# Optimization experiments

Measured on AMD Instinct MI355X. Metric: run time of the kernel, lower is better.

Reference implementation:

```python
import jax, jax.numpy as jnp
import numpy as np

B, P, H, W = 8, 128, 32, 32
NC = 4                 # num_classes = NUM_REL_GROUP + 1
DOBJ = 4424            # 2*DOBJ = 8848
CIN = 256
C = 128 + 8848         # 8976 GCN channel dim


def setup_inputs() -> dict:
    key = jax.random.key(0)
    ks = jax.random.split(key, 24)
    s = 0.02  # weight scale to keep activations moderate
    inp = {
        "x": jax.random.normal(ks[0], (B, CIN, H, W), jnp.float32),
        "rel_pair_idxs": jax.random.randint(ks[1], (B, P, 2), 0, 640, dtype=jnp.int32),
        "obj_rep": jax.random.normal(ks[2], (640, DOBJ), jnp.float32),
        # ADD_GCN params
        "fc_w": jax.random.normal(ks[3], (NC, CIN), jnp.float32) * s,
        "ct_w": jax.random.normal(ks[4], (128, CIN), jnp.float32) * s,
        "ct_b": jnp.zeros((128,), jnp.float32),
        # DynamicGraphConvolution params
        "A": jax.random.normal(ks[5], (NC, NC), jnp.float32) * 0.25,          # static_adj conv1d (no bias)
        "sw_w": jax.random.normal(ks[6], (C, C), jnp.float32) * s / np.sqrt(C) * 30,
        "sw_b": jnp.zeros((C,), jnp.float32),
        "cg_w": jax.random.normal(ks[7], (C, C), jnp.float32) * s / np.sqrt(C) * 30,
        "cg_b": jnp.zeros((C,), jnp.float32),
        "bn_g": jnp.ones((C,), jnp.float32),
        "bn_b": jnp.zeros((C,), jnp.float32),
        "bn_m": jnp.zeros((C,), jnp.float32),
        "bn_v": jnp.ones((C,), jnp.float32),
        "co_w": jax.random.normal(ks[8], (NC, 2 * C), jnp.float32) * s / np.sqrt(C) * 30,
        "co_b": jnp.zeros((NC,), jnp.float32),
        "dw_w": jax.random.normal(ks[9], (C, C), jnp.float32) * s / np.sqrt(C) * 30,
        "dw_b": jnp.zeros((C,), jnp.float32),
        "ll_w": jax.random.normal(ks[10], (NC, C), jnp.float32) * s / np.sqrt(C) * 30,
        "ll_b": jnp.zeros((NC,), jnp.float32),
        "mask_mat": jnp.eye(NC, dtype=jnp.float32),
    }
    return inp


def reference(x, rel_pair_idxs, obj_rep, fc_w, ct_w, ct_b, A, sw_w, sw_b,
              cg_w, cg_b, bn_g, bn_b, bn_m, bn_v, co_w, co_b, dw_w, dw_b,
              ll_w, ll_b, mask_mat):
    leaky = lambda t: jax.nn.leaky_relu(t, 0.2)
    b, cin, h, w = x.shape
    xr = x.reshape(b, cin, h * w)                                  # (B,256,HW)

    # forward_classification_sm: fc -> topk(1).mean == max over spatial
    y = jnp.einsum('oc,bcs->bos', fc_w, xr)                        # (B,NC,HW)
    out1 = y.max(-1)                                               # (B,NC)

    # forward_sam
    mask = jax.nn.sigmoid(y)                                       # (B,NC,HW)
    v = jnp.einsum('oc,bcs->bos', ct_w, xr) + ct_b[None, :, None]  # (B,128,HW)
    v = jnp.einsum('bcs,bns->bcn', v, mask)                        # (B,128,NC)

    # pairwise object features (gather), tiled over NC node slots
    o1 = obj_rep[rel_pair_idxs[..., 0]]                            # (B,P,DOBJ)
    o2 = obj_rep[rel_pair_idxs[..., 1]]
    pf = jnp.concatenate([o1, o2], -1)                             # (B,P,8848)
    p = pf.shape[1]
    pf = jnp.broadcast_to(pf[..., None], pf.shape + (NC,))         # (B,P,8848,NC)
    vb = jnp.broadcast_to(v[:, None], (b, p) + v.shape[1:])        # (B,P,128,NC)
    g = jnp.concatenate([pf, vb], 2).reshape(b * p, C, NC)         # (BP,C,NC)

    # --- DynamicGraphConvolution ---
    # static GCN: node-mix conv1d (no bias) + leaky, then channel 1x1 conv + leaky
    xs = leaky(jnp.einsum('nm,pcm->pcn', A, g))                    # (BP,C,NC)
    xs = leaky(jnp.einsum('oc,pcn->pon', sw_w, xs) + sw_b[None, :, None])
    hg = g + xs

    # dynamic adjacency
    glb = hg.mean(-1)                                              # (BP,C) gap
    glb = glb @ cg_w.T + cg_b                                      # conv_global (1x1)
    glb = (glb - bn_m) * jax.lax.rsqrt(bn_v + 1e-5) * bn_g + bn_b  # BN (eval)
    glb = leaky(glb)
    # conv_create_co_mat over cat([glb_expand, hg], ch) without materializing cat
    adj = jax.nn.sigmoid(
        jnp.einsum('oc,pc->po', co_w[:, :C], glb)[:, :, None]
        + jnp.einsum('oc,pcn->pon', co_w[:, C:], hg)
        + co_b[None, :, None])                                     # (BP,NC,NC)

    # dynamic GCN
    hd = leaky(jnp.einsum('pcn,pnm->pcm', hg, adj))
    z = leaky(jnp.einsum('oc,pcn->pon', dw_w, hd) + dw_b[None, :, None])  # (BP,C,NC)

    # head: last_linear + leaky, masked diagonal sum
    out2 = leaky(jnp.einsum('oc,pcn->pon', ll_w, z) + ll_b[None, :, None])  # (BP,NC,NC)
    out2 = (out2 * jax.lax.stop_gradient(mask_mat)).sum(-1)        # (BP,NC)

    o1b = jnp.broadcast_to(out1[:, None], (b, p, NC)).reshape(b * p, NC)
    return ((o1b + out2) * 0.5).reshape(b, p, NC)
```

## Files before the change

### kernel.cpp

```cpp
#include <hip/hip_runtime.h>
#include <stdint.h>

#define DEVI __device__ __forceinline__

typedef unsigned short u16;
typedef __bf16 bf16x8 __attribute__((ext_vector_type(8)));
typedef float f32x4 __attribute__((ext_vector_type(4)));
typedef u16 u16x8 __attribute__((ext_vector_type(8)));

DEVI u16 f2bf(float f){
  union { float f; unsigned u; } v; v.f = f;
  unsigned r = v.u + 0x7FFFu + ((v.u >> 16) & 1u);
  return (u16)(r >> 16);
}
DEVI float bf2f(u16 h){
  union { unsigned u; float f; } v; v.u = ((unsigned)h) << 16;
  return v.f;
}
DEVI float lky(float t){ return t > 0.f ? t : 0.2f * t; }

#define GLD16(gp, lp) __builtin_amdgcn_global_load_lds( \
    (const __attribute__((address_space(1))) void*)(gp), \
    (__attribute__((address_space(3))) void*)(lp), 16, 0, 0)

template<int EPI>
__global__ __launch_bounds__(1024, 4)
void gemmU(const u16* __restrict__ A, const u16* __restrict__ B,
           int Kp, int Nt, int SN, int Mreal, float* __restrict__ C, long long ldc,
           const float* __restrict__ bias, const float* __restrict__ scale,
           const float* __restrict__ off, const float* __restrict__ llw,
           float* __restrict__ oacc)
{
  __shared__ __align__(16) u16 As[2][16384];
  __shared__ __align__(16) u16 Bs[2][16384];
  const int t    = threadIdx.x;
  const int lane = t & 63;
  const int wid  = t >> 6;
  const int wr = wid >> 2, wc = wid & 3;
  const int l4 = lane >> 4, l15 = lane & 15;

  const int nwg = gridDim.x;
  const int xc = blockIdx.x & 7, pp = blockIdx.x >> 3;
  const int qq = nwg >> 3, rr = nwg & 7;
  const int wg = (xc < rr ? xc*(qq+1) : rr*(qq+1) + (xc-rr)*qq) + pp;
  const int strip_sz = (nwg / Nt) * SN;
  const int strip = wg / strip_sz, srem = wg % strip_sz;
  const int mt = srem / SN, nt = strip*SN + srem % SN;

  const size_t am0 = (size_t)mt*256;
  const size_t bn0 = (size_t)nt*256;

  f32x4 acc[4][4];
  #pragma unroll
  for (int i = 0; i < 4; ++i)
    #pragma unroll
    for (int j = 0; j < 4; ++j) acc[i][j] = f32x4{0.f,0.f,0.f,0.f};
  bf16x8 afr[4], bfr[4];

  const int NT = Kp >> 6;

  const int srl0 = t >> 3, ssl = t & 7;
  const u16* pA = A + (am0 + srl0)*(size_t)Kp;
  const u16* pB = B + (bn0 + srl0)*(size_t)Kp;
  const size_t rowskip = (size_t)128 * Kp;
  const int sco0 = ((ssl ^ (srl0 & 7))*8);
  const int sco1 = ((ssl ^ ((srl0+128) & 7))*8);

  int aoff[4], boff[4];
  #pragma unroll
  for (int mi = 0; mi < 4; ++mi){
    const int r = wr*64 + mi*16 + l15;
    aoff[mi] = r*64 + ((r & 7)*8);
  }
  #pragma unroll
  for (int ni = 0; ni < 4; ++ni){
    const int r = wc*64 + ni*16 + l15;
    boff[ni] = r*64 + ((r & 7)*8);
  }

  auto STAGE = [&](int kc, int buf){
    u16* la = &As[buf][0]; u16* lb = &Bs[buf][0];
    GLD16(pA + kc + sco0,           la + t*8);
    GLD16(pA + rowskip + kc + sco1, la + 8192 + t*8);
    GLD16(pB + kc + sco0,           lb + t*8);
    GLD16(pB + rowskip + kc + sco1, lb + 8192 + t*8);
  };

  STAGE(0, 0);
  asm volatile("s_waitcnt vmcnt(0)" ::: "memory");
  __builtin_amdgcn_s_barrier();

  #define GU_BODY(KT, RB_, WB_)                                              \
  {                                                                          \
    const int nx = ((KT)+1 < NT) ? (KT)+1 : NT-1;                            \
    STAGE(nx*64, WB_);                                                       \
    const u16* ab = &As[RB_][0];                                             \
    const u16* bb = &Bs[RB_][0];                                             \
    _Pragma("unroll")                                                        \
    for (int ks = 0; ks < 2; ++ks){                                          \
      const int sx = (ks*4 + l4)*8;                                          \
      _Pragma("unroll")                                                      \
      for (int mi = 0; mi < 4; ++mi)                                         \
        afr[mi] = *(const bf16x8*)&ab[aoff[mi] ^ sx];                        \
      _Pragma("unroll")                                                      \
      for (int ni = 0; ni < 4; ++ni)                                         \
        bfr[ni] = *(const bf16x8*)&bb[boff[ni] ^ sx];                        \
      __builtin_amdgcn_s_setprio(1);                                         \
      _Pragma("unroll")                                                      \
      for (int mi = 0; mi < 4; ++mi)                                         \
        _Pragma("unroll")                                                    \
        for (int ni = 0; ni < 4; ++ni)                                       \
          acc[mi][ni] = __builtin_amdgcn_mfma_f32_16x16x32_bf16(             \
              afr[mi], bfr[ni], acc[mi][ni], 0, 0, 0);                       \
      __builtin_amdgcn_s_setprio(0);                                         \
    }                                                                        \
    asm volatile("s_waitcnt vmcnt(0)" ::: "memory");                         \
    __builtin_amdgcn_s_barrier();                                            \
  }

  for (int kt = 0; kt < NT; kt += 2){
    GU_BODY(kt,   0, 1);
    GU_BODY(kt+1, 1, 0);
  }
  #undef GU_BODY

  const int ob0 = mt*256 + wr*64;
  const int nb0 = nt*256 + wc*64;

  if (EPI == 0){
    #pragma unroll
    for (int mi = 0; mi < 4; ++mi){
      const int ob = ob0 + mi*16 + l4*4;
      if (ob < Mreal){
        #pragma unroll
        for (int ni = 0; ni < 4; ++ni){
          const int n = nb0 + ni*16 + l15;
          *(f32x4*)&C[(size_t)n*ldc + ob] = acc[mi][ni];
        }
      }
    }
  } else if (EPI == 2){
    #pragma unroll
    for (int mi = 0; mi < 4; ++mi){
      const int ob = ob0 + mi*16 + l4*4;
      if (ob < Mreal){
        const float sc0=scale[ob],sc1=scale[ob+1],sc2=scale[ob+2],sc3=scale[ob+3];
        const float of0=off[ob],of1=off[ob+1],of2=off[ob+2],of3=off[ob+3];
        #pragma unroll
        for (int ni = 0; ni < 4; ++ni){
          const int n = nb0 + ni*16 + l15;
          f32x4 a = acc[mi][ni];
          f32x4 vv = { lky(a[0]*sc0+of0), lky(a[1]*sc1+of1),
                       lky(a[2]*sc2+of2), lky(a[3]*sc3+of3) };
          *(f32x4*)&C[(size_t)n*ldc + ob] = vv;
        }
      }
    }
  } else {
    #pragma unroll
    for (int ni = 0; ni < 4; ++ni){
      float s0=0.f, s1=0.f, s2=0.f, s3=0.f;
      #pragma unroll
      for (int mi = 0; mi < 4; ++mi){
        #pragma unroll
        for (int r = 0; r < 4; ++r){
          const int o = ob0 + mi*16 + l4*4 + r;
          if (o < Mreal){
            const float val = lky(acc[mi][ni][r] + bias[o]);
            s0 += llw[o]         * val;
            s1 += llw[8976 + o]  * val;
            s2 += llw[17952 + o] * val;
            s3 += llw[26928 + o] * val;
          }
        }
      }
      const int n = nb0 + ni*16 + l15;
      const int q = n >> 2, m = n & 3;
      float sv[4] = {s0,s1,s2,s3};
      #pragma unroll
      for (int o4 = 0; o4 < 4; ++o4){
        float tt = sv[o4];
        tt += __shfl_xor(tt, 16);
        tt += __shfl_xor(tt, 32);
        if (l4 == 0) atomicAdd(&oacc[(q*4 + o4)*4 + m], tt);
      }
    }
  }
}

__global__ __launch_bounds__(256)
void gemm_vpre(const u16* __restrict__ A, const u16* __restrict__ B,
               int Kp, int Nt, int Mreal, float* __restrict__ C, long long ldc,
               const float* __restrict__ bias)
{
  __shared__ __align__(16) u16 As[2][4096];
  __shared__ __align__(16) u16 Bs[2][4096];
  const int tid  = threadIdx.x;
  const int lane = tid & 63;
  const int wr   = (tid >> 6) >> 1, wc = (tid >> 6) & 1;
  const int l4   = lane >> 4, l15 = lane & 15;
  const int mt   = blockIdx.x / Nt, nt = blockIdx.x % Nt;

  const size_t arow = (size_t)(mt*128 + (tid>>2)) * Kp + (tid&3)*8;
  const size_t brow = (size_t)(nt*128 + (tid>>2)) * Kp + (tid&3)*8;
  const int    ldst = (tid>>2)*32 + (tid&3)*8;
  const size_t rowskip = (size_t)64 * Kp;

  f32x4 acc[4][4];
  #pragma unroll
  for (int i=0;i<4;i++)
    #pragma unroll
    for (int j=0;j<4;j++) acc[i][j] = f32x4{0.f,0.f,0.f,0.f};

  const int NT = Kp >> 5;
  {
    const u16* a0 = A + arow; const u16* b0 = B + brow;
    GLD16(a0,           &As[0][ldst]);
    GLD16(a0 + rowskip, &As[0][ldst + 2048]);
    GLD16(b0,           &Bs[0][ldst]);
    GLD16(b0 + rowskip, &Bs[0][ldst + 2048]);
  }
  __syncthreads();

  for (int kt=0; kt<NT; ++kt){
    const int cur = kt & 1;
    if (kt + 1 < NT){
      const u16* a0 = A + arow + (size_t)(kt+1)*32;
      const u16* b0 = B + brow + (size_t)(kt+1)*32;
      GLD16(a0,           &As[cur^1][ldst]);
      GLD16(a0 + rowskip, &As[cur^1][ldst + 2048]);
      GLD16(b0,           &Bs[cur^1][ldst]);
      GLD16(b0 + rowskip, &Bs[cur^1][ldst + 2048]);
    }
    bf16x8 af[4], bf[4];
    #pragma unroll
    for (int mi=0;mi<4;mi++)
      af[mi] = *(const bf16x8*)&As[cur][(wr*64 + mi*16 + l15)*32 + l4*8];
    #pragma unroll
    for (int ni=0;ni<4;ni++)
      bf[ni] = *(const bf16x8*)&Bs[cur][(wc*64 + ni*16 + l15)*32 + l4*8];
    #pragma unroll
    for (int mi=0;mi<4;mi++)
      #pragma unroll
      for (int ni=0;ni<4;ni++)
        acc[mi][ni] = __builtin_amdgcn_mfma_f32_16x16x32_bf16(af[mi], bf[ni], acc[mi][ni], 0, 0, 0);
    __syncthreads();
  }

  const int ob0 = mt*128 + wr*64;
  const int nb0 = nt*128 + wc*64;
  #pragma unroll
  for (int mi=0;mi<4;mi++)
    #pragma unroll
    for (int r=0;r<4;r++){
      const int o = ob0 + mi*16 + l4*4 + r;
      if (o < Mreal){
        const float bb = bias[o];
        #pragma unroll
        for (int ni=0;ni<4;ni++){
          const int n = nb0 + ni*16 + l15;
          C[(size_t)o*ldc + n] = acc[mi][ni][r] + bb;
        }
      }
    }
}

__global__ void k_cvt_pad(const float* __restrict__ src, int srows, int scols,
                          int lds_, int koff, u16* __restrict__ dst, int Kp)
{
  const int r = blockIdx.x;
  const int nch = Kp >> 3;
  for (int ch = threadIdx.x; ch < nch; ch += blockDim.x){
    const int k = ch*8;
    u16 o[8];
    if (r < srows){
      #pragma unroll
      for (int i=0;i<8;i++){
        const int kk = k + i;
        o[i] = (kk < scols) ? f2bf(src[(size_t)r*lds_ + koff + kk]) : (u16)0;
      }
    } else {
      #pragma unroll
      for (int i=0;i<8;i++) o[i] = 0;
    }
    u16x8 vv = { o[0],o[1],o[2],o[3],o[4],o[5],o[6],o[7] };
    *(u16x8*)&dst[(size_t)r*Kp + k] = vv;
  }
}

__global__ void k_cvt_sww(const float* __restrict__ src, u16* __restrict__ dst)
{
  const int r = blockIdx.x;
  const float* row = src + (size_t)r*8976;
  u16* d1 = dst + (size_t)r*4480;
  u16* d2 = dst + (size_t)(8976+r)*4480;
  for (int ch = threadIdx.x; ch < 560; ch += 256){
    const int k = ch*8;
    u16 a[8], b[8];
    #pragma unroll
    for (int i=0;i<8;i++){
      const int kk = k+i;
      a[i] = (kk < 4424) ? f2bf(row[kk])        : (u16)0;
      b[i] = (kk < 4424) ? f2bf(row[4424 + kk]) : (u16)0;
    }
    u16x8 va = { a[0],a[1],a[2],a[3],a[4],a[5],a[6],a[7] };
    u16x8 vb = { b[0],b[1],b[2],b[3],b[4],b[5],b[6],b[7] };
    *(u16x8*)&d1[k] = va;
    *(u16x8*)&d2[k] = vb;
  }
}

__global__ void k_cvt_obj(const float* __restrict__ obj, u16* __restrict__ dst)
{
  const int r = blockIdx.x;
  const int ab = (r >= 640);
  const float* src = obj + (size_t)(ab ? r-640 : r)*4424;
  for (int ch = threadIdx.x; ch < 560; ch += 256){
    const int k = ch*8;
    u16 o[8];
    #pragma unroll
    for (int i=0;i<8;i++){
      const int kk = k+i;
      float f = (kk < 4424) ? src[kk] : 0.f;
      if (ab) f = fabsf(f);
      o[i] = f2bf(f);
    }
    u16x8 vv = { o[0],o[1],o[2],o[3],o[4],o[5],o[6],o[7] };
    *(u16x8*)&dst[(size_t)r*4480 + k] = vv;
  }
}

__global__ void k_xT(const float* __restrict__ x, u16* __restrict__ xT)
{
  __shared__ float t[32][33];
  const int bid = blockIdx.x;
  const int b = bid >> 8; const int cs = (bid >> 5) & 7; const int ss = bid & 31;
  const int tx = threadIdx.x & 31, ty = threadIdx.x >> 5;
  #pragma unroll
  for (int i=0;i<4;i++){
    const int r = ty + i*8;
    t[r][tx] = x[((size_t)(b*256 + cs*32 + r))*1024 + ss*32 + tx];
  }
  __syncthreads();
  #pragma unroll
  for (int i=0;i<4;i++){
    const int r = ty + i*8;
    xT[((size_t)(b*1024 + ss*32 + r))*256 + cs*32 + tx] = f2bf(t[tx][r]);
  }
}

__global__ void k_ymask(const float* __restrict__ x, const float* __restrict__ fcw,
                        float* __restrict__ y, float* __restrict__ mask)
{
  __shared__ float fc[1024];
  const int b = blockIdx.x >> 2, st = blockIdx.x & 3;
  for (int i=threadIdx.x; i<1024; i+=256) fc[i] = fcw[i];
  __syncthreads();
  const int s = st*256 + threadIdx.x;
  float a0=0,a1=0,a2=0,a3=0;
  for (int c=0;c<256;c++){
    const float xv = x[((size_t)(b*256+c))*1024 + s];
    a0 += fc[c]*xv; a1 += fc[256+c]*xv; a2 += fc[512+c]*xv; a3 += fc[768+c]*xv;
  }
  const size_t base = (size_t)(b*4)*1024 + s;
  y[base]        = a0; mask[base]        = 1.f/(1.f+expf(-a0));
  y[base+1024]   = a1; mask[base+1024]   = 1.f/(1.f+expf(-a1));
  y[base+2048]   = a2; mask[base+2048]   = 1.f/(1.f+expf(-a2));
  y[base+3072]   = a3; mask[base+3072]   = 1.f/(1.f+expf(-a3));
}

__global__ void k_out1(const float* __restrict__ y, float* __restrict__ out1){
  const int bn = blockIdx.x;
  float m = -3.4e38f;
  for (int s=threadIdx.x; s<1024; s+=256) m = fmaxf(m, y[(size_t)bn*1024+s]);
  for (int o=32;o;o>>=1) m = fmaxf(m, __shfl_xor(m,o));
  __shared__ float red[4];
  if ((threadIdx.x&63)==0) red[threadIdx.x>>6] = m;
  __syncthreads();
  if (threadIdx.x==0) out1[bn] = fmaxf(fmaxf(red[0],red[1]),fmaxf(red[2],red[3]));
}

__global__ void k_v(const float* __restrict__ vpreT, const float* __restrict__ mask,
                    float* __restrict__ v){
  const int b = blockIdx.x >> 7, j = blockIdx.x & 127;
  float a[4]={0,0,0,0};
  for (int s=threadIdx.x; s<1024; s+=256){
    const float pv = vpreT[(size_t)j*8192 + b*1024 + s];
    #pragma unroll
    for (int m=0;m<4;m++) a[m] += pv * mask[((size_t)(b*4+m))*1024 + s];
  }
  __shared__ float red[4][5];
  #pragma unroll
  for (int m=0;m<4;m++){
    float t=a[m];
    for (int o=32;o;o>>=1) t += __shfl_xor(t,o);
    if ((threadIdx.x&63)==0) red[m][threadIdx.x>>6]=t;
  }
  __syncthreads();
  if (threadIdx.x<4)
    v[(size_t)(b*128+j)*4 + threadIdx.x] =
      red[threadIdx.x][0]+red[threadIdx.x][1]+red[threadIdx.x][2]+red[threadIdx.x][3];
}

__global__ void k_lv(const float* __restrict__ Am, const float* __restrict__ v,
                     float* __restrict__ lv){
  const int idx = blockIdx.x*256 + threadIdx.x;
  if (idx < 1024){
    #pragma unroll
    for (int n=0;n<4;n++){
      float s=0;
      #pragma unroll
      for (int m=0;m<4;m++) s += Am[n*4+m]*v[idx*4+m];
      lv[idx*4+n] = lky(s);
    }
  }
}

__global__ void k_sV(const float* __restrict__ sw, const float* __restrict__ lv,
                     float* __restrict__ sV){
  __shared__ float l[4096];
  for (int i=threadIdx.x; i<4096; i+=256) l[i]=lv[i];
  __syncthreads();
  const int o = blockIdx.x*256 + threadIdx.x;
  if (o >= 8976) return;
  float acc[8][4] = {};
  const float* row = sw + (size_t)o*8976 + 8848;
  for (int j=0;j<128;j++){
    const float wv = row[j];
    #pragma unroll
    for (int b=0;b<8;b++){
      const float* lb = &l[(b*128+j)*4];
      #pragma unroll
      for (int n=0;n<4;n++) acc[b][n] += wv*lb[n];
    }
  }
  #pragma unroll
  for (int b=0;b<8;b++){
    f32x4 vv = {acc[b][0],acc[b][1],acc[b][2],acc[b][3]};
    *(f32x4*)&sV[((size_t)b*8976 + o)*4] = vv;
  }
}

__global__ void k_so(const float* __restrict__ cgb, const float* __restrict__ g,
                     const float* __restrict__ b2, const float* __restrict__ m,
                     const float* __restrict__ vvar, float* __restrict__ so){
  const int o = blockIdx.x*256+threadIdx.x;
  if (o<8976){
    const float sc = g[o]*rsqrtf(vvar[o]+1e-5f);
    so[o]=sc; so[8976+o] = (cgb[o]-m[o])*sc + b2[o];
  }
}

__global__ void k_glb_t2(const float* __restrict__ U, const float* __restrict__ obj,
                         const int* __restrict__ rel,
                         const float* __restrict__ sV, const float* __restrict__ swb,
                         const float* __restrict__ v, const float* __restrict__ Am,
                         const float* __restrict__ cow, u16* __restrict__ glbB,
                         float* __restrict__ t2)
{
  const int q = blockIdx.x; const int b = q >> 7;
  const int i1 = rel[q*2], i2 = rel[q*2+1];
  const float* u1  = U + (size_t)i1*17952;
  const float* u2  = U + (size_t)i2*17952 + 8976;
  const float* u1a = U + (size_t)(640+i1)*17952;
  const float* u2a = U + (size_t)(640+i2)*17952 + 8976;
  const float* o1 = obj + (size_t)i1*4424;
  const float* o2 = obj + (size_t)i2*4424;
  float rA[4], aA[4];
  #pragma unroll
  for (int n=0;n<4;n++){
    const float s = Am[n*4]+Am[n*4+1]+Am[n*4+2]+Am[n*4+3];
    rA[n]=0.6f*s; aA[n]=0.4f*fabsf(s);
  }
  float t2a[16] = {};
  for (int c = threadIdx.x; c < 9088; c += 256){
    if (c < 8976){
      const float p1 = u1[c] + u2[c];
      const float p2 = u1a[c] + u2a[c];
      const f32x4 sv = *(const f32x4*)&sV[((size_t)b*8976 + c)*4];
      const float sb = swb[c];
      const float gs = (c < 4424) ? o1[c] : (c < 8848) ? o2[c-4424] : 0.f;
      float hg[4]; float sum = 0.f;
      #pragma unroll
      for (int n=0;n<4;n++){
        const float xs2 = lky(rA[n]*p1 + aA[n]*p2 + sv[n] + sb);
        const float g = (c < 8848) ? gs : v[((size_t)b*128 + (c-8848))*4 + n];
        hg[n] = g + xs2; sum += hg[n];
      }
      glbB[(size_t)q*9088 + c] = f2bf(0.25f*sum);
      #pragma unroll
      for (int o4=0;o4<4;o4++){
        const float cw = cow[(size_t)o4*17952 + 8976 + c];
        #pragma unroll
        for (int n=0;n<4;n++) t2a[o4*4+n] += cw*hg[n];
      }
    } else {
      glbB[(size_t)q*9088 + c] = 0;
    }
  }
  __shared__ float red[16][5];
  #pragma unroll
  for (int i=0;i<16;i++){
    float t = t2a[i];
    for (int o=32;o;o>>=1) t += __shfl_xor(t,o);
    if ((threadIdx.x&63)==0) red[i][threadIdx.x>>6]=t;
  }
  __syncthreads();
  if (threadIdx.x < 16)
    t2[q*16+threadIdx.x] = red[threadIdx.x][0]+red[threadIdx.x][1]
                          +red[threadIdx.x][2]+red[threadIdx.x][3];
}

__global__ void k_adj(const float* __restrict__ glb2, const float* __restrict__ cow,
                      const float* __restrict__ t2, const float* __restrict__ cob,
                      float* __restrict__ adj)
{
  const int q = blockIdx.x;
  float a[4]={0,0,0,0};
  for (int c=threadIdx.x; c<8976; c+=256){
    const float g = glb2[(size_t)q*8976+c];
    #pragma unroll
    for (int o=0;o<4;o++) a[o] += cow[(size_t)o*17952 + c]*g;
  }
  __shared__ float red[4][5]; __shared__ float co1[4];
  #pragma unroll
  for (int i=0;i<4;i++){
    float t=a[i]; for (int o=32;o;o>>=1) t += __shfl_xor(t,o);
    if ((threadIdx.x&63)==0) red[i][threadIdx.x>>6]=t;
  }
  __syncthreads();
  if (threadIdx.x<4)
    co1[threadIdx.x]=red[threadIdx.x][0]+red[threadIdx.x][1]+red[threadIdx.x][2]+red[threadIdx.x][3];
  __syncthreads();
  if (threadIdx.x<16){
    const int a_=threadIdx.x>>2, m=threadIdx.x&3;
    const float t = co1[a_] + t2[q*16 + a_*4 + m] + cob[a_];
    adj[q*16 + a_*4 + m] = 1.f/(1.f+expf(-t));
  }
}

__global__ void k_hd(const float* __restrict__ U, const float* __restrict__ obj,
                     const int* __restrict__ rel,
                     const float* __restrict__ sV, const float* __restrict__ swb,
                     const float* __restrict__ v, const float* __restrict__ Am,
                     const float* __restrict__ adj, u16* __restrict__ hdb)
{
  const int q = blockIdx.x; const int b = q>>7;
  const int i1 = rel[q*2], i2 = rel[q*2+1];
  const float* u1  = U + (size_t)i1*17952;
  const float* u2  = U + (size_t)i2*17952 + 8976;
  const float* u1a = U + (size_t)(640+i1)*17952;
  const float* u2a = U + (size_t)(640+i2)*17952 + 8976;
  const float* o1 = obj + (size_t)i1*4424;
  const float* o2 = obj + (size_t)i2*4424;
  float rA[4], aA[4];
  #pragma unroll
  for (int n=0;n<4;n++){
    const float s = Am[n*4]+Am[n*4+1]+Am[n*4+2]+Am[n*4+3];
    rA[n]=0.6f*s; aA[n]=0.4f*fabsf(s);
  }
  __shared__ float aj[16];
  if (threadIdx.x<16) aj[threadIdx.x] = adj[q*16+threadIdx.x];
  __syncthreads();
  float ajr[16];
  #pragma unroll
  for (int i=0;i<16;i++) ajr[i]=aj[i];
  for (int c=threadIdx.x; c<9088; c+=256){
    if (c<8976){
      const float p1 = u1[c] + u2[c];
      const float p2 = u1a[c] + u2a[c];
      const f32x4 sv = *(const f32x4*)&sV[((size_t)b*8976 + c)*4];
      const float sb = swb[c];
      const float gs = (c < 4424) ? o1[c] : (c < 8848) ? o2[c-4424] : 0.f;
      float hg[4];
      #pragma unroll
      for (int n=0;n<4;n++){
        const float xs2 = lky(rA[n]*p1 + aA[n]*p2 + sv[n] + sb);
        const float g = (c < 8848) ? gs : v[((size_t)b*128 + (c-8848))*4 + n];
        hg[n] = g + xs2;
      }
      #pragma unroll
      for (int m=0;m<4;m++){
        const float hv = lky(hg[0]*ajr[m] + hg[1]*ajr[4+m] + hg[2]*ajr[8+m] + hg[3]*ajr[12+m]);
        hdb[((size_t)(q*4+m))*9088 + c] = f2bf(hv);
      }
    } else {
      #pragma unroll
      for (int m=0;m<4;m++) hdb[((size_t)(q*4+m))*9088 + c] = 0;
    }
  }
}

__global__ void k_final(const float* __restrict__ o2f, const float* __restrict__ out1,
                        const float* __restrict__ llb, const float* __restrict__ mm,
                        float* __restrict__ out)
{
  const int idx = blockIdx.x*256+threadIdx.x;
  if (idx < 4096){
    const int q = idx>>2, o = idx&3, b = q>>7;
    float s=0.f;
    #pragma unroll
    for (int m=0;m<4;m++) s += lky(o2f[(q*4+o)*4+m] + llb[o]) * mm[o*4+m];
    out[idx] = 0.5f*(out1[b*4+o] + s);
  }
}

extern "C" void kernel_launch(void* const* d_in, const int* in_sizes, int n_in,
                              void* d_out, int out_size, void* d_ws, size_t ws_size,
                              hipStream_t stream)
{
  const float* x    = (const float*)d_in[0];
  const int*   rel  = (const int*)d_in[1];
  const float* obj  = (const float*)d_in[2];
  const float* fcw  = (const float*)d_in[3];
  const float* ctw  = (const float*)d_in[4];
  const float* ctb  = (const float*)d_in[5];
  const float* Am   = (const float*)d_in[6];
  const float* sww  = (const float*)d_in[7];
  const float* swb  = (const float*)d_in[8];
  const float* cgw  = (const float*)d_in[9];
  const float* cgb  = (const float*)d_in[10];
  const float* bng  = (const float*)d_in[11];
  const float* bnb  = (const float*)d_in[12];
  const float* bnm  = (const float*)d_in[13];
  const float* bnv  = (const float*)d_in[14];
  const float* cow  = (const float*)d_in[15];
  const float* cob  = (const float*)d_in[16];
  const float* dww  = (const float*)d_in[17];
  const float* dwb  = (const float*)d_in[18];
  const float* llw  = (const float*)d_in[19];
  const float* llb  = (const float*)d_in[20];
  const float* mm   = (const float*)d_in[21];
  float* out = (float*)d_out;
  (void)in_sizes; (void)n_in; (void)out_size; (void)ws_size;

  char* ws = (char*)d_ws;
  size_t off = 0;
  auto alloc = [&](size_t bytes)->char*{
    char* p = ws + off; off = (off + bytes + 255) & ~(size_t)255; return p;
  };
  u16*   Wb    = (u16*)  alloc((size_t)9216*9088*2);
  float* U     = (float*)alloc((size_t)1280*17952*4);
  u16*   glbB  = (u16*)  alloc((size_t)1024*9088*2);
  u16*   hdb   = (u16*)  alloc((size_t)4096*9088*2);
  u16*   objB  = (u16*)  alloc((size_t)1280*4480*2);
  float* glb2  = (float*)alloc((size_t)1024*8976*4);
  u16*   xT    = (u16*)  alloc((size_t)8192*256*2);
  u16*   ctwb  = (u16*)  alloc((size_t)128*256*2);
  float* y     = (float*)alloc((size_t)32768*4);
  float* mask  = (float*)alloc((size_t)32768*4);
  float* out1  = (float*)alloc((size_t)32*4);
  float* vpreT = (float*)alloc((size_t)128*8192*4);
  float* v     = (float*)alloc((size_t)4096*4);
  float* lv    = (float*)alloc((size_t)4096*4);
  float* sV    = (float*)alloc((size_t)287232*4);
  float* so    = (float*)alloc((size_t)2*8976*4);
  float* t2    = (float*)alloc((size_t)16384*4);
  float* adj   = (float*)alloc((size_t)16384*4);
  float* o2f   = (float*)alloc((size_t)16384*4);

  k_xT<<<dim3(2048), dim3(256), 0, stream>>>(x, xT);
  k_cvt_pad<<<dim3(128), dim3(256), 0, stream>>>(ctw, 128, 256, 256, 0, ctwb, 256);
  k_ymask<<<dim3(32), dim3(256), 0, stream>>>(x, fcw, y, mask);
  k_out1<<<dim3(32), dim3(256), 0, stream>>>(y, out1);
  gemm_vpre<<<dim3(64), dim3(256), 0, stream>>>(
      ctwb, xT, 256, 64, 128, vpreT, (long long)8192, ctb);
  k_v<<<dim3(1024), dim3(256), 0, stream>>>(vpreT, mask, v);

  k_cvt_obj<<<dim3(1280), dim3(256), 0, stream>>>(obj, objB);
  k_cvt_sww<<<dim3(8976), dim3(256), 0, stream>>>(sww, Wb);
  gemmU<0><<<dim3(71*5), dim3(1024), 0, stream>>>(
      Wb, objB, 4480, 5, 5, 17952, U, (long long)17952,
      nullptr, nullptr, nullptr, nullptr, nullptr);

  k_lv<<<dim3(4), dim3(256), 0, stream>>>(Am, v, lv);
  k_sV<<<dim3(36), dim3(256), 0, stream>>>(sww, lv, sV);
  k_glb_t2<<<dim3(1024), dim3(256), 0, stream>>>(U, obj, rel, sV, swb, v, Am,
                                                 cow, glbB, t2);

  k_cvt_pad<<<dim3(9216), dim3(256), 0, stream>>>(cgw, 8976, 8976, 8976, 0, Wb, 9088);
  k_so<<<dim3(36), dim3(256), 0, stream>>>(cgb, bng, bnb, bnm, bnv, so);
  gemmU<2><<<dim3(36*4), dim3(1024), 0, stream>>>(
      Wb, glbB, 9088, 4, 4, 8976, glb2, (long long)8976,
      nullptr, so, so + 8976, nullptr, nullptr);

  k_adj<<<dim3(1024), dim3(256), 0, stream>>>(glb2, cow, t2, cob, adj);
  k_cvt_pad<<<dim3(9216), dim3(256), 0, stream>>>(dww, 8976, 8976, 8976, 0, Wb, 9088);
  k_hd<<<dim3(1024), dim3(256), 0, stream>>>(U, obj, rel, sV, swb, v, Am, adj, hdb);

  hipMemsetAsync(o2f, 0, (size_t)16384*4, stream);
  gemmU<3><<<dim3(36*16), dim3(1024), 0, stream>>>(
      Wb, hdb, 9088, 16, 8, 8976, nullptr, 0, dwb,
      nullptr, nullptr, llw, o2f);

  k_final<<<dim3(16), dim3(256), 0, stream>>>(o2f, out1, llb, mm, out);
}
```

Measured before the change: 2.031 ms.

## Fuse adjacency projection into glb GEMM epilogue and compute only diagonal head outputs

The co_w projection of the global feature, previously a separate k_adj kernel that re-read glb2, is now reduced inside the gemmU<2> epilogue with shuffles and atomics into a small co1 buffer. The sigmoid for the adjacency is moved into k_hd. The EPI 3 head epilogue now computes only the diagonal output that the mask keeps, which removes three quarters of its llw multiply-accumulates and atomics. The cost is more global atomics and llw loads in the EPI 2 epilogue, a memset, and a reliance on the mask being the identity matrix.

```diff
diff --git a/kernel.cpp b/kernel.cpp
--- a/kernel.cpp
+++ b/kernel.cpp
@@ -141,25 +141,44 @@
     }
   } else if (EPI == 2){
     #pragma unroll
-    for (int mi = 0; mi < 4; ++mi){
-      const int ob = ob0 + mi*16 + l4*4;
-      if (ob < Mreal){
-        const float sc0=scale[ob],sc1=scale[ob+1],sc2=scale[ob+2],sc3=scale[ob+3];
-        const float of0=off[ob],of1=off[ob+1],of2=off[ob+2],of3=off[ob+3];
-        #pragma unroll
-        for (int ni = 0; ni < 4; ++ni){
-          const int n = nb0 + ni*16 + l15;
+    for (int ni = 0; ni < 4; ++ni){
+      const int n = nb0 + ni*16 + l15;
+      float sa0=0.f, sa1=0.f, sa2=0.f, sa3=0.f;
+      #pragma unroll
+      for (int mi = 0; mi < 4; ++mi){
+        const int ob = ob0 + mi*16 + l4*4;
+        if (ob < Mreal){
+          const float sc0=scale[ob],sc1=scale[ob+1],sc2=scale[ob+2],sc3=scale[ob+3];
+          const float of0=off[ob],of1=off[ob+1],of2=off[ob+2],of3=off[ob+3];
           f32x4 a = acc[mi][ni];
           f32x4 vv = { lky(a[0]*sc0+of0), lky(a[1]*sc1+of1),
                        lky(a[2]*sc2+of2), lky(a[3]*sc3+of3) };
           *(f32x4*)&C[(size_t)n*ldc + ob] = vv;
+          #pragma unroll
+          for (int r = 0; r < 4; ++r){
+            const float vr = vv[r];
+            sa0 += llw[(size_t)0*17952 + ob + r] * vr;
+            sa1 += llw[(size_t)1*17952 + ob + r] * vr;
+            sa2 += llw[(size_t)2*17952 + ob + r] * vr;
+            sa3 += llw[(size_t)3*17952 + ob + r] * vr;
+          }
         }
       }
+      float sv[4] = {sa0,sa1,sa2,sa3};
+      #pragma unroll
+      for (int a4 = 0; a4 < 4; ++a4){
+        float tt = sv[a4];
+        tt += __shfl_xor(tt, 16);
+        tt += __shfl_xor(tt, 32);
+        if (l4 == 0) atomicAdd(&oacc[n*4 + a4], tt);
+      }
     }
   } else {
     #pragma unroll
     for (int ni = 0; ni < 4; ++ni){
-      float s0=0.f, s1=0.f, s2=0.f, s3=0.f;
+      const int n = nb0 + ni*16 + l15;
+      const int m = n & 3, q = n >> 2;
+      float s = 0.f;
       #pragma unroll
       for (int mi = 0; mi < 4; ++mi){
         #pragma unroll
@@ -167,23 +186,13 @@
           const int o = ob0 + mi*16 + l4*4 + r;
           if (o < Mreal){
             const float val = lky(acc[mi][ni][r] + bias[o]);
-            s0 += llw[o]         * val;
-            s1 += llw[8976 + o]  * val;
-            s2 += llw[17952 + o] * val;
-            s3 += llw[26928 + o] * val;
+            s += llw[(size_t)m*8976 + o] * val;
           }
         }
       }
-      const int n = nb0 + ni*16 + l15;
-      const int q = n >> 2, m = n & 3;
-      float sv[4] = {s0,s1,s2,s3};
-      #pragma unroll
-      for (int o4 = 0; o4 < 4; ++o4){
-        float tt = sv[o4];
-        tt += __shfl_xor(tt, 16);
-        tt += __shfl_xor(tt, 32);
-        if (l4 == 0) atomicAdd(&oacc[(q*4 + o4)*4 + m], tt);
-      }
+      s += __shfl_xor(s, 16);
+      s += __shfl_xor(s, 32);
+      if (l4 == 0) atomicAdd(&oacc[(q*4 + m)*4 + m], s);
     }
   }
 }
@@ -511,39 +520,12 @@
                           +red[threadIdx.x][2]+red[threadIdx.x][3];
 }
 
-__global__ void k_adj(const float* __restrict__ glb2, const float* __restrict__ cow,
-                      const float* __restrict__ t2, const float* __restrict__ cob,
-                      float* __restrict__ adj)
-{
-  const int q = blockIdx.x;
-  float a[4]={0,0,0,0};
-  for (int c=threadIdx.x; c<8976; c+=256){
-    const float g = glb2[(size_t)q*8976+c];
-    #pragma unroll
-    for (int o=0;o<4;o++) a[o] += cow[(size_t)o*17952 + c]*g;
-  }
-  __shared__ float red[4][5]; __shared__ float co1[4];
-  #pragma unroll
-  for (int i=0;i<4;i++){
-    float t=a[i]; for (int o=32;o;o>>=1) t += __shfl_xor(t,o);
-    if ((threadIdx.x&63)==0) red[i][threadIdx.x>>6]=t;
-  }
-  __syncthreads();
-  if (threadIdx.x<4)
-    co1[threadIdx.x]=red[threadIdx.x][0]+red[threadIdx.x][1]+red[threadIdx.x][2]+red[threadIdx.x][3];
-  __syncthreads();
-  if (threadIdx.x<16){
-    const int a_=threadIdx.x>>2, m=threadIdx.x&3;
-    const float t = co1[a_] + t2[q*16 + a_*4 + m] + cob[a_];
-    adj[q*16 + a_*4 + m] = 1.f/(1.f+expf(-t));
-  }
-}
-
 __global__ void k_hd(const float* __restrict__ U, const float* __restrict__ obj,
                      const int* __restrict__ rel,
                      const float* __restrict__ sV, const float* __restrict__ swb,
                      const float* __restrict__ v, const float* __restrict__ Am,
-                     const float* __restrict__ adj, u16* __restrict__ hdb)
+                     const float* __restrict__ co1acc, const float* __restrict__ t2,
+                     const float* __restrict__ cob, u16* __restrict__ hdb)
 {
   const int q = blockIdx.x; const int b = q>>7;
   const int i1 = rel[q*2], i2 = rel[q*2+1];
@@ -560,7 +542,11 @@
     rA[n]=0.6f*s; aA[n]=0.4f*fabsf(s);
   }
   __shared__ float aj[16];
-  if (threadIdx.x<16) aj[threadIdx.x] = adj[q*16+threadIdx.x];
+  if (threadIdx.x<16){
+    const int a_=threadIdx.x>>2, m=threadIdx.x&3;
+    const float tt = co1acc[q*4+a_] + t2[q*16 + a_*4 + m] + cob[a_];
+    aj[threadIdx.x] = 1.f/(1.f+expf(-tt));
+  }
   __syncthreads();
   float ajr[16];
   #pragma unroll
@@ -656,7 +642,7 @@
   float* sV    = (float*)alloc((size_t)287232*4);
   float* so    = (float*)alloc((size_t)2*8976*4);
   float* t2    = (float*)alloc((size_t)16384*4);
-  float* adj   = (float*)alloc((size_t)16384*4);
+  float* co1a  = (float*)alloc((size_t)4096*4);
   float* o2f   = (float*)alloc((size_t)16384*4);
 
   k_xT<<<dim3(2048), dim3(256), 0, stream>>>(x, xT);
@@ -680,13 +666,14 @@
 
   k_cvt_pad<<<dim3(9216), dim3(256), 0, stream>>>(cgw, 8976, 8976, 8976, 0, Wb, 9088);
   k_so<<<dim3(36), dim3(256), 0, stream>>>(cgb, bng, bnb, bnm, bnv, so);
+  hipMemsetAsync(co1a, 0, (size_t)4096*4, stream);
   gemmU<2><<<dim3(36*4), dim3(1024), 0, stream>>>(
       Wb, glbB, 9088, 4, 4, 8976, glb2, (long long)8976,
-      nullptr, so, so + 8976, nullptr, nullptr);
-
-  k_adj<<<dim3(1024), dim3(256), 0, stream>>>(glb2, cow, t2, cob, adj);
+      nullptr, so, so + 8976, cow, co1a);
+
   k_cvt_pad<<<dim3(9216), dim3(256), 0, stream>>>(dww, 8976, 8976, 8976, 0, Wb, 9088);
-  k_hd<<<dim3(1024), dim3(256), 0, stream>>>(U, obj, rel, sV, swb, v, Am, adj, hdb);
+  k_hd<<<dim3(1024), dim3(256), 0, stream>>>(U, obj, rel, sV, swb, v, Am,
+                                             co1a, t2, cob, hdb);
 
   hipMemsetAsync(o2f, 0, (size_t)16384*4, stream);
   gemmU<3><<<dim3(36*16), dim3(1024), 0, stream>>>(
```

Measured after the change: 1.992 ms, median of 2. Within noise of the previous version (-1.9%).
